# Kernel tuning notes

Hardware: AMD Instinct MI355X
Metric: run time of the kernel (lower is better)

Reference implementation:

```python
import jax, jax.numpy as jnp
import numpy as np

H = 16       # query heads
KV = 4       # kv heads
BASE = 10000.0


def _rope(seq_len, head_dim, dtype):
    inv_freq = 1.0 / (BASE ** (jnp.arange(0, head_dim, 2, dtype=jnp.float32) / head_dim))
    t = jnp.arange(seq_len, dtype=jnp.float32)
    freqs = jnp.einsum('i,j->ij', t, inv_freq)          # [S, D/2]
    emb = jnp.concatenate([freqs, freqs], axis=-1)      # [S, D]
    return jnp.cos(emb).astype(dtype), jnp.sin(emb).astype(dtype)


def _rotate_half(x):
    x1, x2 = jnp.split(x, 2, axis=-1)
    return jnp.concatenate([-x2, x1], axis=-1)


def setup_inputs() -> dict:
    key = jax.random.key(0)
    ks = jax.random.split(key, 5)
    B, S, E = 2, 2048, 1024
    return {
        'x': jax.random.normal(ks[0], (B, S, E), jnp.float32),
        'wq': jax.random.normal(ks[1], (E, E), jnp.float32) * (E ** -0.5),
        'wk': jax.random.normal(ks[2], (KV * (E // H), E), jnp.float32) * (E ** -0.5),
        'wv': jax.random.normal(ks[3], (KV * (E // H), E), jnp.float32) * (E ** -0.5),
        'wo': jax.random.normal(ks[4], (E, E), jnp.float32) * (E ** -0.5),
    }


def reference(x, wq, wk, wv, wo):
    B, S, E = x.shape
    D = E // H
    G = H // KV  # query heads per kv head
    scale = D ** -0.5

    q = (x @ wq.T).reshape(B, S, H, D).transpose(0, 2, 1, 3)    # [B,H,S,D]
    k = (x @ wk.T).reshape(B, S, KV, D).transpose(0, 2, 1, 3)   # [B,KV,S,D]
    v = (x @ wv.T).reshape(B, S, KV, D).transpose(0, 2, 1, 3)   # [B,KV,S,D]

    cos, sin = _rope(S, D, x.dtype)                              # [S,D] each
    q = q * cos + _rotate_half(q) * sin
    k = k * cos + _rotate_half(k) * sin

    # GQA: group query heads per kv head instead of materializing repeated K/V
    qg = q.reshape(B, KV, G, S, D)
    scores = jnp.einsum('bkgsd,bktd->bkgst', qg, k) * scale      # [B,KV,G,S,S]
    causal = jnp.triu(jnp.ones((S, S), dtype=bool), k=1)
    scores = jnp.where(causal, jnp.finfo(scores.dtype).min, scores)
    attn = jax.nn.softmax(scores, axis=-1)
    out = jnp.einsum('bkgst,bktd->bkgsd', attn, v)               # [B,KV,G,S,D]
    out = out.reshape(B, H, S, D).transpose(0, 2, 1, 3).reshape(B, S, E)
    return out @ wo.T
```

## Files before the change

### kernel.cpp

```cpp
#include <hip/hip_runtime.h>
#include <stdint.h>

typedef unsigned short u16;
typedef __attribute__((ext_vector_type(8))) short s16x8;
typedef __attribute__((ext_vector_type(4))) float f32x4;
typedef __attribute__((ext_vector_type(4))) unsigned short u16x4;
typedef __attribute__((ext_vector_type(2))) unsigned int u32x2;


__device__ __forceinline__ u16 f2bf(float f) {
  unsigned u = __float_as_uint(f);
  unsigned r = (u + 0x7fffu + ((u >> 16) & 1u)) >> 16;
  return (u16)r;
}
__device__ __forceinline__ unsigned cvt_pk(float lo, float hi) {
  unsigned r;
  asm("v_cvt_pk_bf16_f32 %0, %1, %2" : "=v"(r) : "v"(lo), "v"(hi));
  return r;
}
__device__ __forceinline__ float exp2fast(float x) {
  return __builtin_amdgcn_exp2f(x);
}

typedef const __attribute__((address_space(1))) unsigned int* gas_ptr;
typedef __attribute__((address_space(3))) unsigned int* las_ptr;

__device__ __forceinline__ void g2l16(const void* g, void* l) {
  __builtin_amdgcn_global_load_lds((gas_ptr)g, (las_ptr)l, 16, 0, 0);
}

__device__ __forceinline__ void cvt4(const float* __restrict__ in, u16* __restrict__ out) {
  const f32x4 v = *(const f32x4*)in;
  u16x4 o;
  o[0] = f2bf(v[0]); o[1] = f2bf(v[1]); o[2] = f2bf(v[2]); o[3] = f2bf(v[3]);
  *(u16x4*)out = o;
}


__global__ void prep_kernel(const float* __restrict__ x,  const float* __restrict__ wq,
                            const float* __restrict__ wk, const float* __restrict__ wv,
                            const float* __restrict__ wo,
                            u16* __restrict__ xb, u16* __restrict__ wcat, u16* __restrict__ wob,
                            float* __restrict__ cosT, float* __restrict__ sinT) {
  const long id = (long)blockIdx.x * 256 + threadIdx.x;
  if (id < 262144) {
    cvt4(wq + id * 4, wcat + id * 4);
  } else if (id < 327680) {
    const long i = id - 262144;
    cvt4(wk + i * 4, wcat + 1048576 + i * 4);
  } else if (id < 393216) {
    const long i = id - 327680;
    cvt4(wv + i * 4, wcat + 1310720 + i * 4);
  } else if (id < 655360) {
    const long i = id - 393216;
    cvt4(wo + i * 4, wob + i * 4);
  } else if (id < 671744) {
    const long t = id - 655360;
#pragma unroll
    for (int u = 0; u < 4; ++u) {
      const long idx = t * 4 + u;
      const int s = (int)(idx >> 5), j = (int)(idx & 31);
      const double invd = exp(-(double)j * 0.2878231366242558);
      const float a = (float)s * (float)invd;
      cosT[idx] = cosf(a);
      sinT[idx] = sinf(a);
    }
  } else {
    const long i = id - 671744;
    cvt4(x + i * 4, xb + i * 4);
  }
}


__global__ __launch_bounds__(256, 2) void gemm_qkv_kernel(
    const u16* __restrict__ A, const u16* __restrict__ W,
    u16* __restrict__ qo, u16* __restrict__ ko, u16* __restrict__ vto,
    const float* __restrict__ cosT, const float* __restrict__ sinT) {
  const int K = 1024;
  __shared__ __align__(16) u16 As[2][128 * 64];
  __shared__ __align__(16) u16 Bs[2][128 * 64];
  const int tid = threadIdx.x;
  const int lane = tid & 63;
  const int wave = tid >> 6;
  const int g = lane >> 4, l15 = lane & 15;
  const int wr = wave >> 1, wc = wave & 1;
  const int bid = blockIdx.x;
  const int arowBlk = (bid & 7) * 4 + ((bid >> 3) & 3);
  const int wcolBlk = bid >> 5;
  const long arow0 = (long)arowBlk * 128;
  const long wrow0 = (long)wcolBlk * 128;
  const u16* Ab = A + arow0 * K;
  const u16* Wb = W + wrow0 * K;
  const bool isV = (wcolBlk >= 10);

  auto STAGE = [&](int buf, int k0) {
#pragma unroll
    for (int i = 0; i < 4; ++i) {
      const int lbase = i * 256 + wave * 64;
      const int c = lbase + lane;
      const int r = c >> 3, c8 = c & 7;
      const int cs = (c8 ^ (r & 7)) * 8;
      g2l16(Ab + (long)r * K + k0 + cs, (char*)As[buf] + lbase * 16);
      g2l16(Wb + (long)r * K + k0 + cs, (char*)Bs[buf] + lbase * 16);
    }
  };

  f32x4 acc[4][4] = {};
  int cur = 0;
  STAGE(0, 0);

  for (int k0 = 0; k0 < K; k0 += 64) {
    if (k0 + 64 < K) {
      STAGE(cur ^ 1, k0 + 64);
      asm volatile("s_waitcnt vmcnt(8)" ::: "memory");
    } else {
      asm volatile("s_waitcnt vmcnt(0)" ::: "memory");
    }
    __builtin_amdgcn_s_barrier();
#pragma unroll
    for (int ks = 0; ks < 2; ++ks) {
      s16x8 af[4], bfr[4];
#pragma unroll
      for (int m = 0; m < 4; ++m) {
        const int row = wr * 64 + m * 16 + l15;
        af[m] = *(const s16x8*)((const char*)As[cur] + row * 128 + (((ks * 4 + g) ^ (row & 7)) << 4));
      }
#pragma unroll
      for (int n = 0; n < 4; ++n) {
        const int row = wc * 64 + n * 16 + l15;
        bfr[n] = *(const s16x8*)((const char*)Bs[cur] + row * 128 + (((ks * 4 + g) ^ (row & 7)) << 4));
      }
      __builtin_amdgcn_s_setprio(1);
      if (!isV) {
#pragma unroll
        for (int m = 0; m < 4; ++m)
#pragma unroll
          for (int n = 0; n < 4; ++n)
            acc[m][n] = __builtin_amdgcn_mfma_f32_16x16x32_bf16(af[m], bfr[n], acc[m][n], 0, 0, 0);
      } else {
#pragma unroll
        for (int m = 0; m < 4; ++m)
#pragma unroll
          for (int n = 0; n < 4; ++n)
            acc[m][n] = __builtin_amdgcn_mfma_f32_16x16x32_bf16(bfr[m], af[n], acc[m][n], 0, 0, 0);
      }
      __builtin_amdgcn_s_setprio(0);
    }
    __builtin_amdgcn_s_barrier();
    cur ^= 1;
  }

  const int colBase = (int)wrow0 + wc * 64;
  const int j0 = l15;
  const float QSCALE = 0.18033688011112042f;

  if (colBase < 1024) {
    const int h2 = colBase >> 6;
#pragma unroll
    for (int m = 0; m < 4; ++m) {
      const int grow = (int)arow0 + wr * 64 + m * 16 + g * 4;
#pragma unroll
      for (int r = 0; r < 4; ++r) {
        const int row = grow + r;
        const int s = row & 2047, bb = row >> 11;
        const long ob = (((long)(bb * 16 + h2)) * 2048 + s) * 64;
        const float c0 = cosT[s * 32 + j0],      s0 = sinT[s * 32 + j0];
        const float c1 = cosT[s * 32 + 16 + j0], s1 = sinT[s * 32 + 16 + j0];
        qo[ob + j0]      = f2bf((acc[m][0][r] * c0 - acc[m][2][r] * s0) * QSCALE);
        qo[ob + 16 + j0] = f2bf((acc[m][1][r] * c1 - acc[m][3][r] * s1) * QSCALE);
        qo[ob + 32 + j0] = f2bf((acc[m][2][r] * c0 + acc[m][0][r] * s0) * QSCALE);
        qo[ob + 48 + j0] = f2bf((acc[m][3][r] * c1 + acc[m][1][r] * s1) * QSCALE);
      }
    }
  } else if (colBase < 1280) {
    const int kvh2 = (colBase - 1024) >> 6;
#pragma unroll
    for (int m = 0; m < 4; ++m) {
      const int grow = (int)arow0 + wr * 64 + m * 16 + g * 4;
#pragma unroll
      for (int r = 0; r < 4; ++r) {
        const int row = grow + r;
        const int s = row & 2047, bb = row >> 11;
        const long ob = (((long)(bb * 4 + kvh2)) * 2048 + s) * 64;
        const float c0 = cosT[s * 32 + j0],      s0 = sinT[s * 32 + j0];
        const float c1 = cosT[s * 32 + 16 + j0], s1 = sinT[s * 32 + 16 + j0];
        ko[ob + j0]      = f2bf(acc[m][0][r] * c0 - acc[m][2][r] * s0);
        ko[ob + 16 + j0] = f2bf(acc[m][1][r] * c1 - acc[m][3][r] * s1);
        ko[ob + 32 + j0] = f2bf(acc[m][2][r] * c0 + acc[m][0][r] * s0);
        ko[ob + 48 + j0] = f2bf(acc[m][3][r] * c1 + acc[m][1][r] * s1);
      }
    }
  } else {
    const int kvh2 = (colBase - 1280) >> 6;
    const int bb = (int)(arow0 >> 11);
    const int sBase = (int)(arow0 & 2047) + wr * 64;
    const long vrow0 = ((long)(bb * 4 + kvh2)) * 64;
#pragma unroll
    for (int mw = 0; mw < 4; ++mw) {
      const int d0 = mw * 16 + g * 4;
#pragma unroll
      for (int r = 0; r < 4; ++r) {
        const long db = (vrow0 + d0 + r) * 2048;
#pragma unroll
        for (int nx = 0; nx < 4; ++nx)
          vto[db + sBase + nx * 16 + l15] = f2bf(acc[mw][nx][r]);
      }
    }
  }
}


__global__ __launch_bounds__(256, 2) void gemm_out_kernel(
    const u16* __restrict__ A, const u16* __restrict__ W, float* __restrict__ Y) {
  const int K = 1024, N = 1024;
  __shared__ __align__(16) u16 As[2][128 * 64];
  __shared__ __align__(16) u16 Bs[2][128 * 64];
  const int tid = threadIdx.x;
  const int lane = tid & 63;
  const int wave = tid >> 6;
  const int g = lane >> 4, l15 = lane & 15;
  const int wr = wave >> 1, wc = wave & 1;
  const int bid = blockIdx.x;
  const int arowBlk = (bid & 7) * 4 + ((bid >> 3) & 3);
  const int wcolBlk = bid >> 5;
  const long arow0 = (long)arowBlk * 128;
  const long wrow0 = (long)wcolBlk * 128;
  const u16* Ab = A + arow0 * K;
  const u16* Wb = W + wrow0 * K;

  auto STAGE = [&](int buf, int k0) {
#pragma unroll
    for (int i = 0; i < 4; ++i) {
      const int lbase = i * 256 + wave * 64;
      const int c = lbase + lane;
      const int r = c >> 3, c8 = c & 7;
      const int cs = (c8 ^ (r & 7)) * 8;
      g2l16(Ab + (long)r * K + k0 + cs, (char*)As[buf] + lbase * 16);
      g2l16(Wb + (long)r * K + k0 + cs, (char*)Bs[buf] + lbase * 16);
    }
  };

  f32x4 acc[4][4] = {};
  int cur = 0;
  STAGE(0, 0);

  for (int k0 = 0; k0 < K; k0 += 64) {
    if (k0 + 64 < K) {
      STAGE(cur ^ 1, k0 + 64);
      asm volatile("s_waitcnt vmcnt(8)" ::: "memory");
    } else {
      asm volatile("s_waitcnt vmcnt(0)" ::: "memory");
    }
    __builtin_amdgcn_s_barrier();
#pragma unroll
    for (int ks = 0; ks < 2; ++ks) {
      s16x8 af[4], bfr[4];
#pragma unroll
      for (int m = 0; m < 4; ++m) {
        const int row = wr * 64 + m * 16 + l15;
        af[m] = *(const s16x8*)((const char*)As[cur] + row * 128 + (((ks * 4 + g) ^ (row & 7)) << 4));
      }
#pragma unroll
      for (int n = 0; n < 4; ++n) {
        const int row = wc * 64 + n * 16 + l15;
        bfr[n] = *(const s16x8*)((const char*)Bs[cur] + row * 128 + (((ks * 4 + g) ^ (row & 7)) << 4));
      }
      __builtin_amdgcn_s_setprio(1);
#pragma unroll
      for (int m = 0; m < 4; ++m)
#pragma unroll
        for (int n = 0; n < 4; ++n)
          acc[m][n] = __builtin_amdgcn_mfma_f32_16x16x32_bf16(af[m], bfr[n], acc[m][n], 0, 0, 0);
      __builtin_amdgcn_s_setprio(0);
    }
    __builtin_amdgcn_s_barrier();
    cur ^= 1;
  }

#pragma unroll
  for (int m = 0; m < 4; ++m)
#pragma unroll
    for (int n = 0; n < 4; ++n) {
      const long gr0 = arow0 + wr * 64 + m * 16 + g * 4;
      const long gc = wrow0 + wc * 64 + n * 16 + l15;
#pragma unroll
      for (int r = 0; r < 4; ++r)
        Y[(gr0 + r) * N + gc] = acc[m][n][r];
    }
}


__global__ __launch_bounds__(256, 3) void flash_kernel(
    const u16* __restrict__ qg,
    const u16* __restrict__ kg,
    const u16* __restrict__ vtg,
    u16* __restrict__ og) {
  const int tid = threadIdx.x, lane = tid & 63, w = tid >> 6;
  const int g = lane >> 4, l15 = lane & 15;

  const int bid = blockIdx.x;
  const int lid = (bid & 7) * 128 + (bid >> 3);
  const int qtIdx = lid & 31;
  const int h = (lid >> 5) & 15;
  const int b = lid >> 9;
  const int qt = (qtIdx & 1) ? (31 - (qtIdx >> 1)) : (qtIdx >> 1);
  const int kvh = h >> 2;

  __shared__ __align__(16) u16 Kl[2][64 * 64];
  __shared__ __align__(16) u16 Vl[2][64 * 64];
  __shared__ __align__(16) u16 Pl[4][16][72];

  const u16* Kp = kg  + ((long)(b * 4 + kvh)) * 2048 * 64;
  const u16* Vp = vtg + ((long)(b * 4 + kvh)) * 64 * 2048;

  auto STAGE = [&](int buf, int kt) {
#pragma unroll
    for (int j = 0; j < 2; ++j) {
      const int lbase = j * 256 + w * 64;
      const int c = lbase + lane;
      const int row = c >> 3, c8 = c & 7;
      const int cs = (c8 ^ (row & 7)) * 8;
      g2l16(Kp + ((long)(kt * 64 + row)) * 64 + cs, (char*)Kl[buf] + lbase * 16);
      g2l16(Vp + (long)row * 2048 + kt * 64 + cs,  (char*)Vl[buf] + lbase * 16);
    }
  };

  const u16* Qp = qg + (((long)(b * 16 + h)) * 2048 + qt * 64 + w * 16) * 64;
  const s16x8 qf0 = *(const s16x8*)(Qp + l15 * 64 + g * 8);
  const s16x8 qf1 = *(const s16x8*)(Qp + l15 * 64 + 32 + g * 8);

  f32x4 of[4] = {};
  float m = -1e30f, lsum = 0.f;
  const int qrow = qt * 64 + w * 16 + l15;

  int cur = 0;
  STAGE(0, 0);

#pragma unroll 1
  for (int kt = 0; kt <= qt; ++kt) {
    if (kt < qt) {
      STAGE(cur ^ 1, kt + 1);
      asm volatile("s_waitcnt vmcnt(4)" ::: "memory");
    } else {
      asm volatile("s_waitcnt vmcnt(0)" ::: "memory");
    }
    __builtin_amdgcn_s_barrier();
    const u16* Kb = Kl[cur];
    const u16* Vb = Vl[cur];

    f32x4 sf[4] = {};
    __builtin_amdgcn_s_setprio(1);
#pragma unroll
    for (int ks = 0; ks < 2; ++ks) {
      const s16x8 qv = ks ? qf1 : qf0;
#pragma unroll
      for (int fn = 0; fn < 4; ++fn) {
        const int row = fn * 16 + l15;
        const s16x8 kf = *(const s16x8*)((const char*)Kb + row * 128 + (((ks * 4 + g) ^ (row & 7)) << 4));
        sf[fn] = __builtin_amdgcn_mfma_f32_16x16x32_bf16(kf, qv, sf[fn], 0, 0, 0);
      }
    }
    __builtin_amdgcn_s_setprio(0);

    const bool diag = (kt == qt);
    float p[16];
#pragma unroll
    for (int fn = 0; fn < 4; ++fn)
#pragma unroll
      for (int r = 0; r < 4; ++r) {
        float sv = sf[fn][r];
        if (diag) {
          const int kv = kt * 64 + fn * 16 + 4 * g + r;
          if (kv > qrow) sv = -1e30f;
        }
        p[fn * 4 + r] = sv;
      }
    const float t0 = fmaxf(fmaxf(p[0], p[1]), p[2]);
    const float t1 = fmaxf(fmaxf(p[3], p[4]), p[5]);
    const float t2 = fmaxf(fmaxf(p[6], p[7]), p[8]);
    const float t3 = fmaxf(fmaxf(p[9], p[10]), p[11]);
    const float t4 = fmaxf(fmaxf(p[12], p[13]), p[14]);
    float mx = fmaxf(fmaxf(fmaxf(t0, t1), t2), fmaxf(fmaxf(t3, t4), p[15]));
    mx = fmaxf(mx, __shfl_xor(mx, 16));
    mx = fmaxf(mx, __shfl_xor(mx, 32));

    if (!__all(mx - m <= 11.0f)) {
      const float mn = fmaxf(m, mx);
      const float al = exp2fast(m - mn);
      m = mn;
      lsum *= al;
      float alq[4];
#pragma unroll
      for (int r = 0; r < 4; ++r) alq[r] = __shfl(al, 4 * g + r);
#pragma unroll
      for (int fd = 0; fd < 4; ++fd)
#pragma unroll
        for (int r = 0; r < 4; ++r) of[fd][r] *= alq[r];
    }

#pragma unroll
    for (int i = 0; i < 16; ++i) p[i] = exp2fast(p[i] - m);
    const float s0 = (p[0] + p[1]) + (p[2] + p[3]);
    const float s1 = (p[4] + p[5]) + (p[6] + p[7]);
    const float s2 = (p[8] + p[9]) + (p[10] + p[11]);
    const float s3 = (p[12] + p[13]) + (p[14] + p[15]);
    float rs = (s0 + s1) + (s2 + s3);
    rs += __shfl_xor(rs, 16);
    rs += __shfl_xor(rs, 32);
    lsum += rs;

    u16* Pw = &Pl[w][l15][0];
#pragma unroll
    for (int fn = 0; fn < 4; ++fn) {
      const u32x2 v2 = {cvt_pk(p[fn * 4 + 0], p[fn * 4 + 1]),
                        cvt_pk(p[fn * 4 + 2], p[fn * 4 + 3])};
      *(u32x2*)(Pw + fn * 16 + g * 4) = v2;
    }

    __builtin_amdgcn_s_setprio(1);
#pragma unroll
    for (int ks = 0; ks < 2; ++ks) {
      const s16x8 pa = *(const s16x8*)(&Pl[w][l15][ks * 32 + g * 8]);
#pragma unroll
      for (int fd = 0; fd < 4; ++fd) {
        const int vrow = fd * 16 + l15;
        const s16x8 vf = *(const s16x8*)((const char*)Vb + vrow * 128 + (((ks * 4 + g) ^ (vrow & 7)) << 4));
        of[fd] = __builtin_amdgcn_mfma_f32_16x16x32_bf16(pa, vf, of[fd], 0, 0, 0);
      }
    }
    __builtin_amdgcn_s_setprio(0);

    __builtin_amdgcn_s_barrier();
    cur ^= 1;
  }

  float linv[4];
#pragma unroll
  for (int r = 0; r < 4; ++r) linv[r] = 1.0f / __shfl(lsum, 4 * g + r);
  const long orow0 = (long)b * 2048 + qt * 64 + w * 16 + 4 * g;
#pragma unroll
  for (int r = 0; r < 4; ++r) {
    const long gb = (orow0 + r) * 1024 + h * 64;
#pragma unroll
    for (int fd = 0; fd < 4; ++fd)
      og[gb + fd * 16 + l15] = f2bf(of[fd][r] * linv[r]);
  }
}


extern "C" void kernel_launch(void* const* d_in, const int* in_sizes, int n_in,
                              void* d_out, int out_size, void* d_ws, size_t ws_size,
                              hipStream_t stream) {
  (void)in_sizes; (void)n_in; (void)out_size; (void)ws_size;
  const float* x  = (const float*)d_in[0];
  const float* wq = (const float*)d_in[1];
  const float* wk = (const float*)d_in[2];
  const float* wv = (const float*)d_in[3];
  const float* wo = (const float*)d_in[4];
  float* out = (float*)d_out;

  char* p = (char*)d_ws;
  auto alloc = [&](size_t bytes) { char* r = p; p += (bytes + 255) & ~(size_t)255; return r; };

  u16* xb    = (u16*)alloc(4096ull * 1024 * 2);
  u16* wcat  = (u16*)alloc(1536ull * 1024 * 2);
  u16* wob   = (u16*)alloc(1024ull * 1024 * 2);
  u16* qrb   = (u16*)alloc(4096ull * 1024 * 2);
  u16* krb   = (u16*)alloc(4096ull * 256 * 2);
  u16* vtb   = (u16*)alloc(4096ull * 256 * 2);
  u16* aob   = (u16*)alloc(4096ull * 1024 * 2);
  float* cosT = (float*)alloc(2048ull * 32 * 4);
  float* sinT = (float*)alloc(2048ull * 32 * 4);

  prep_kernel<<<6720, 256, 0, stream>>>(x, wq, wk, wv, wo, xb, wcat, wob, cosT, sinT);

  gemm_qkv_kernel<<<384, 256, 0, stream>>>(xb, wcat, qrb, krb, vtb, cosT, sinT);

  flash_kernel<<<1024, 256, 0, stream>>>(qrb, krb, vtb, aob);

  gemm_out_kernel<<<256, 256, 0, stream>>>(aob, wob, out);
}
```

Baseline: 194.0 us.

## Pair causal query tiles per block, triple-buffer K/V, swizzle P tile

Each flash-attention block now handles two query tiles, qt and 31-qt, one after the other. Every block therefore does the same amount of causal work, and the grid is halved to 512 blocks with launch bounds of 2 blocks per CU. K/V staging in LDS moves from double to triple buffering, which drops the trailing barrier in each iteration so only one barrier per KV tile remains. The per-wave P scratch loses its padding and uses an XOR swizzle instead. In exchange, more LDS per block and fewer resident blocks could reduce latency hiding.

```diff
diff --git a/kernel.cpp b/kernel.cpp
--- a/kernel.cpp
+++ b/kernel.cpp
@@ -290,7 +290,7 @@
 }
 
 
-__global__ __launch_bounds__(256, 3) void flash_kernel(
+__global__ __launch_bounds__(256, 2) void flash_kernel(
     const u16* __restrict__ qg,
     const u16* __restrict__ kg,
     const u16* __restrict__ vtg,
@@ -299,16 +299,13 @@
   const int g = lane >> 4, l15 = lane & 15;
 
   const int bid = blockIdx.x;
-  const int lid = (bid & 7) * 128 + (bid >> 3);
-  const int qtIdx = lid & 31;
-  const int h = (lid >> 5) & 15;
-  const int b = lid >> 9;
-  const int qt = (qtIdx & 1) ? (31 - (qtIdx >> 1)) : (qtIdx >> 1);
+  const int lid = (bid & 7) * 64 + (bid >> 3);
+  const int pr = lid & 15, h = (lid >> 4) & 15, b = lid >> 8;
   const int kvh = h >> 2;
 
-  __shared__ __align__(16) u16 Kl[2][64 * 64];
-  __shared__ __align__(16) u16 Vl[2][64 * 64];
-  __shared__ __align__(16) u16 Pl[4][16][72];
+  __shared__ __align__(16) u16 Kl[3][64 * 64];
+  __shared__ __align__(16) u16 Vl[3][64 * 64];
+  __shared__ __align__(16) u16 Pl[4][16 * 64];
 
   const u16* Kp = kg  + ((long)(b * 4 + kvh)) * 2048 * 64;
   const u16* Vp = vtg + ((long)(b * 4 + kvh)) * 64 * 2048;
@@ -325,125 +322,131 @@
     }
   };
 
-  const u16* Qp = qg + (((long)(b * 16 + h)) * 2048 + qt * 64 + w * 16) * 64;
-  const s16x8 qf0 = *(const s16x8*)(Qp + l15 * 64 + g * 8);
-  const s16x8 qf1 = *(const s16x8*)(Qp + l15 * 64 + 32 + g * 8);
-
-  f32x4 of[4] = {};
-  float m = -1e30f, lsum = 0.f;
-  const int qrow = qt * 64 + w * 16 + l15;
-
-  int cur = 0;
-  STAGE(0, 0);
-
 #pragma unroll 1
-  for (int kt = 0; kt <= qt; ++kt) {
-    if (kt < qt) {
-      STAGE(cur ^ 1, kt + 1);
-      asm volatile("s_waitcnt vmcnt(4)" ::: "memory");
-    } else {
-      asm volatile("s_waitcnt vmcnt(0)" ::: "memory");
-    }
-    __builtin_amdgcn_s_barrier();
-    const u16* Kb = Kl[cur];
-    const u16* Vb = Vl[cur];
-
-    f32x4 sf[4] = {};
-    __builtin_amdgcn_s_setprio(1);
-#pragma unroll
-    for (int ks = 0; ks < 2; ++ks) {
-      const s16x8 qv = ks ? qf1 : qf0;
+  for (int pass = 0; pass < 2; ++pass) {
+    const int qt = pass ? (31 - pr) : pr;
+    const u16* Qp = qg + (((long)(b * 16 + h)) * 2048 + qt * 64 + w * 16) * 64;
+    const s16x8 qf0 = *(const s16x8*)(Qp + l15 * 64 + g * 8);
+    const s16x8 qf1 = *(const s16x8*)(Qp + l15 * 64 + 32 + g * 8);
+
+    f32x4 of[4] = {};
+    float m = -1e30f, lsum = 0.f;
+    const int qrow = qt * 64 + w * 16 + l15;
+
+    int cb = 0;
+    STAGE(0, 0);
+
+#pragma unroll 1
+    for (int kt = 0; kt <= qt; ++kt) {
+      const int nb = (cb == 2) ? 0 : cb + 1;
+      if (kt < qt) {
+        STAGE(nb, kt + 1);
+        asm volatile("s_waitcnt vmcnt(4)" ::: "memory");
+      } else {
+        asm volatile("s_waitcnt vmcnt(0)" ::: "memory");
+      }
+      __builtin_amdgcn_s_barrier();
+      const u16* Kb = Kl[cb];
+      const u16* Vb = Vl[cb];
+
+      f32x4 sf[4] = {};
+      __builtin_amdgcn_s_setprio(1);
+#pragma unroll
+      for (int ks = 0; ks < 2; ++ks) {
+        const s16x8 qv = ks ? qf1 : qf0;
+#pragma unroll
+        for (int fn = 0; fn < 4; ++fn) {
+          const int row = fn * 16 + l15;
+          const s16x8 kf = *(const s16x8*)((const char*)Kb + row * 128 + (((ks * 4 + g) ^ (row & 7)) << 4));
+          sf[fn] = __builtin_amdgcn_mfma_f32_16x16x32_bf16(kf, qv, sf[fn], 0, 0, 0);
+        }
+      }
+      __builtin_amdgcn_s_setprio(0);
+
+      const bool diag = (kt == qt);
+      float p[16];
+#pragma unroll
+      for (int fn = 0; fn < 4; ++fn)
+#pragma unroll
+        for (int r = 0; r < 4; ++r) {
+          float sv = sf[fn][r];
+          if (diag) {
+            const int kv = kt * 64 + fn * 16 + 4 * g + r;
+            if (kv > qrow) sv = -1e30f;
+          }
+          p[fn * 4 + r] = sv;
+        }
+      const float t0 = fmaxf(fmaxf(p[0], p[1]), p[2]);
+      const float t1 = fmaxf(fmaxf(p[3], p[4]), p[5]);
+      const float t2 = fmaxf(fmaxf(p[6], p[7]), p[8]);
+      const float t3 = fmaxf(fmaxf(p[9], p[10]), p[11]);
+      const float t4 = fmaxf(fmaxf(p[12], p[13]), p[14]);
+      float mx = fmaxf(fmaxf(fmaxf(t0, t1), t2), fmaxf(fmaxf(t3, t4), p[15]));
+      mx = fmaxf(mx, __shfl_xor(mx, 16));
+      mx = fmaxf(mx, __shfl_xor(mx, 32));
+
+      if (!__all(mx - m <= 11.0f)) {
+        const float mn = fmaxf(m, mx);
+        const float al = exp2fast(m - mn);
+        m = mn;
+        lsum *= al;
+        float alq[4];
+#pragma unroll
+        for (int r = 0; r < 4; ++r) alq[r] = __shfl(al, 4 * g + r);
+#pragma unroll
+        for (int fd = 0; fd < 4; ++fd)
+#pragma unroll
+          for (int r = 0; r < 4; ++r) of[fd][r] *= alq[r];
+      }
+
+#pragma unroll
+      for (int i = 0; i < 16; ++i) p[i] = exp2fast(p[i] - m);
+      const float s0 = (p[0] + p[1]) + (p[2] + p[3]);
+      const float s1 = (p[4] + p[5]) + (p[6] + p[7]);
+      const float s2 = (p[8] + p[9]) + (p[10] + p[11]);
+      const float s3 = (p[12] + p[13]) + (p[14] + p[15]);
+      float rs = (s0 + s1) + (s2 + s3);
+      rs += __shfl_xor(rs, 16);
+      rs += __shfl_xor(rs, 32);
+      lsum += rs;
+
+      char* Pw = (char*)Pl[w] + l15 * 128;
 #pragma unroll
       for (int fn = 0; fn < 4; ++fn) {
-        const int row = fn * 16 + l15;
-        const s16x8 kf = *(const s16x8*)((const char*)Kb + row * 128 + (((ks * 4 + g) ^ (row & 7)) << 4));
-        sf[fn] = __builtin_amdgcn_mfma_f32_16x16x32_bf16(kf, qv, sf[fn], 0, 0, 0);
-      }
-    }
-    __builtin_amdgcn_s_setprio(0);
-
-    const bool diag = (kt == qt);
-    float p[16];
-#pragma unroll
-    for (int fn = 0; fn < 4; ++fn)
-#pragma unroll
-      for (int r = 0; r < 4; ++r) {
-        float sv = sf[fn][r];
-        if (diag) {
-          const int kv = kt * 64 + fn * 16 + 4 * g + r;
-          if (kv > qrow) sv = -1e30f;
+        const u32x2 v2 = {cvt_pk(p[fn * 4 + 0], p[fn * 4 + 1]),
+                          cvt_pk(p[fn * 4 + 2], p[fn * 4 + 3])};
+        *(u32x2*)(Pw + ((((2 * fn + (g >> 1)) ^ (l15 & 7))) << 4) + ((g & 1) * 8)) = v2;
+      }
+
+      __builtin_amdgcn_s_setprio(1);
+#pragma unroll
+      for (int ks = 0; ks < 2; ++ks) {
+        const s16x8 pa = *(const s16x8*)(Pw + (((ks * 4 + g) ^ (l15 & 7)) << 4));
+#pragma unroll
+        for (int fd = 0; fd < 4; ++fd) {
+          const int vrow = fd * 16 + l15;
+          const s16x8 vf = *(const s16x8*)((const char*)Vb + vrow * 128 + (((ks * 4 + g) ^ (vrow & 7)) << 4));
+          of[fd] = __builtin_amdgcn_mfma_f32_16x16x32_bf16(pa, vf, of[fd], 0, 0, 0);
         }
-        p[fn * 4 + r] = sv;
-      }
-    const float t0 = fmaxf(fmaxf(p[0], p[1]), p[2]);
-    const float t1 = fmaxf(fmaxf(p[3], p[4]), p[5]);
-    const float t2 = fmaxf(fmaxf(p[6], p[7]), p[8]);
-    const float t3 = fmaxf(fmaxf(p[9], p[10]), p[11]);
-    const float t4 = fmaxf(fmaxf(p[12], p[13]), p[14]);
-    float mx = fmaxf(fmaxf(fmaxf(t0, t1), t2), fmaxf(fmaxf(t3, t4), p[15]));
-    mx = fmaxf(mx, __shfl_xor(mx, 16));
-    mx = fmaxf(mx, __shfl_xor(mx, 32));
-
-    if (!__all(mx - m <= 11.0f)) {
-      const float mn = fmaxf(m, mx);
-      const float al = exp2fast(m - mn);
-      m = mn;
-      lsum *= al;
-      float alq[4];
-#pragma unroll
-      for (int r = 0; r < 4; ++r) alq[r] = __shfl(al, 4 * g + r);
+      }
+      __builtin_amdgcn_s_setprio(0);
+
+      cb = nb;
+    }
+
+    __syncthreads();
+
+    float linv[4];
+#pragma unroll
+    for (int r = 0; r < 4; ++r) linv[r] = 1.0f / __shfl(lsum, 4 * g + r);
+    const long orow0 = (long)b * 2048 + qt * 64 + w * 16 + 4 * g;
+#pragma unroll
+    for (int r = 0; r < 4; ++r) {
+      const long gb = (orow0 + r) * 1024 + h * 64;
 #pragma unroll
       for (int fd = 0; fd < 4; ++fd)
-#pragma unroll
-        for (int r = 0; r < 4; ++r) of[fd][r] *= alq[r];
-    }
-
-#pragma unroll
-    for (int i = 0; i < 16; ++i) p[i] = exp2fast(p[i] - m);
-    const float s0 = (p[0] + p[1]) + (p[2] + p[3]);
-    const float s1 = (p[4] + p[5]) + (p[6] + p[7]);
-    const float s2 = (p[8] + p[9]) + (p[10] + p[11]);
-    const float s3 = (p[12] + p[13]) + (p[14] + p[15]);
-    float rs = (s0 + s1) + (s2 + s3);
-    rs += __shfl_xor(rs, 16);
-    rs += __shfl_xor(rs, 32);
-    lsum += rs;
-
-    u16* Pw = &Pl[w][l15][0];
-#pragma unroll
-    for (int fn = 0; fn < 4; ++fn) {
-      const u32x2 v2 = {cvt_pk(p[fn * 4 + 0], p[fn * 4 + 1]),
-                        cvt_pk(p[fn * 4 + 2], p[fn * 4 + 3])};
-      *(u32x2*)(Pw + fn * 16 + g * 4) = v2;
-    }
-
-    __builtin_amdgcn_s_setprio(1);
-#pragma unroll
-    for (int ks = 0; ks < 2; ++ks) {
-      const s16x8 pa = *(const s16x8*)(&Pl[w][l15][ks * 32 + g * 8]);
-#pragma unroll
-      for (int fd = 0; fd < 4; ++fd) {
-        const int vrow = fd * 16 + l15;
-        const s16x8 vf = *(const s16x8*)((const char*)Vb + vrow * 128 + (((ks * 4 + g) ^ (vrow & 7)) << 4));
-        of[fd] = __builtin_amdgcn_mfma_f32_16x16x32_bf16(pa, vf, of[fd], 0, 0, 0);
-      }
-    }
-    __builtin_amdgcn_s_setprio(0);
-
-    __builtin_amdgcn_s_barrier();
-    cur ^= 1;
-  }
-
-  float linv[4];
-#pragma unroll
-  for (int r = 0; r < 4; ++r) linv[r] = 1.0f / __shfl(lsum, 4 * g + r);
-  const long orow0 = (long)b * 2048 + qt * 64 + w * 16 + 4 * g;
-#pragma unroll
-  for (int r = 0; r < 4; ++r) {
-    const long gb = (orow0 + r) * 1024 + h * 64;
-#pragma unroll
-    for (int fd = 0; fd < 4; ++fd)
-      og[gb + fd * 16 + l15] = f2bf(of[fd][r] * linv[r]);
+        og[gb + fd * 16 + l15] = f2bf(of[fd][r] * linv[r]);
+    }
   }
 }
 
@@ -476,7 +479,7 @@
 
   gemm_qkv_kernel<<<384, 256, 0, stream>>>(xb, wcat, qrb, krb, vtb, cosT, sinT);
 
-  flash_kernel<<<1024, 256, 0, stream>>>(qrb, krb, vtb, aob);
+  flash_kernel<<<512, 256, 0, stream>>>(qrb, krb, vtb, aob);
 
   gemm_out_kernel<<<256, 256, 0, stream>>>(aob, wob, out);
 }
```

After: 166.9 us. 1.16x faster.
